# Kernel tuning notes

Measured on AMD Instinct MI355X. Metric: run time of the kernel, lower is better.

## Reference

```python
import jax, jax.numpy as jnp
import numpy as np

EPS = 1e-5
H = 8  # num_heads


def _layernorm(x, g, b):
    m = x.mean(axis=-1, keepdims=True)
    v = jnp.mean((x - m) ** 2, axis=-1, keepdims=True)
    return (x - m) / jnp.sqrt(v + EPS) * g + b


def setup_inputs() -> dict:
    key = jax.random.key(0)
    ks = jax.random.split(key, 8)
    B, T, N, D, L = 4, 4096, 512, 1024, 768
    x = jax.random.normal(ks[0], (B, T, D), dtype=jnp.float32)
    cond = jax.random.normal(ks[1], (B, N, L), dtype=jnp.float32)
    # LayerNorm params
    ln_g = jnp.ones((D,), jnp.float32)
    ln_b = jnp.zeros((D,), jnp.float32)
    tln_g = jnp.ones((L,), jnp.float32)
    tln_b = jnp.zeros((L,), jnp.float32)
    # Linear params, stored as (in, out)
    Wq = jax.random.normal(ks[2], (D, D), jnp.float32) * 0.02
    bq = jnp.zeros((D,), jnp.float32)
    Wk = jax.random.normal(ks[3], (L, D), jnp.float32) * 0.02
    bk = jnp.zeros((D,), jnp.float32)
    Wv = jax.random.normal(ks[4], (L, D), jnp.float32) * 0.02
    bv = jnp.zeros((D,), jnp.float32)
    return {"input_tensor": x, "condition_tensor": cond,
            "ln_g": ln_g, "ln_b": ln_b, "tln_g": tln_g, "tln_b": tln_b,
            "Wq": Wq, "bq": bq, "Wk": Wk, "bk": bk, "Wv": Wv, "bv": bv}


def reference(input_tensor, condition_tensor, ln_g, ln_b, tln_g, tln_b,
              Wq, bq, Wk, bk, Wv, bv):
    B, T, D = input_tensor.shape
    N = condition_tensor.shape[1]
    xn = _layernorm(input_tensor, ln_g, ln_b)            # [B,T,D]
    cn = _layernorm(condition_tensor, tln_g, tln_b)      # [B,N,L]
    q = jnp.einsum('btd,de->bte', xn, Wq) + bq           # [B,T,D]
    k = jnp.einsum('bnl,ld->bnd', cn, Wk) + bk           # [B,N,D]
    v = jnp.einsum('bnl,ld->bnd', cn, Wv) + bv           # [B,N,D]
    q = jax.nn.softmax(q.reshape(B, T, H, D // H), axis=-1)  # softmax over head_dim
    k = jax.nn.softmax(k.reshape(B, N, H, D // H), axis=1)   # softmax over N
    v = v.reshape(B, N, H, D // H)
    context = jnp.einsum('bnhk,bnhv->bhkv', k, v)        # [B,H,hd,hd]
    y = jnp.einsum('bthk,bhkv->bthv', q, context).reshape(B, T, D)
    return y
```

## Files before the change

kernel.cpp:

```cpp
#include <hip/hip_runtime.h>
#include <hip/hip_bf16.h>
#include <stdint.h>

#define BATCH 4
#define TLEN  4096
#define DDIM  1024
#define NCOND 512
#define LDIM  768
#define NHEAD 8
#define HD    128

typedef __bf16 bf16x8 __attribute__((ext_vector_type(8)));
typedef float  f32x4  __attribute__((ext_vector_type(4)));

__device__ __forceinline__ unsigned short f2b(float f) {
    unsigned int u = __builtin_bit_cast(unsigned int, f);
    unsigned int r = (u + 0x7fffu + ((u >> 16) & 1u)) >> 16;
    return (unsigned short)r;
}
__device__ __forceinline__ float b2f(unsigned short s) {
    unsigned int u = ((unsigned int)s) << 16;
    return __builtin_bit_cast(float, u);
}

__device__ __forceinline__ void gl2lds(const void* g, void* l) {
    __builtin_amdgcn_global_load_lds(
        (const __attribute__((address_space(1))) void*)(uintptr_t)g,
        (__attribute__((address_space(3))) void*)(uintptr_t)l,
        16, 0, 0);
}

template<int NCH>
__global__ __launch_bounds__(256) void ln_apply(const float* __restrict__ x,
    const float* __restrict__ g, const float* __restrict__ bb,
    unsigned short* __restrict__ o, int rowlen)
{
    int wid = threadIdx.x >> 6, lane = threadIdx.x & 63;
    long r = (long)blockIdx.x * 4 + wid;
    const float* p = x + r * (long)rowlen;
    float4 v[NCH];
    float s = 0.f, ss = 0.f;
#pragma unroll
    for (int i = 0; i < NCH; i++) {
        v[i] = *(const float4*)(p + i * 256 + lane * 4);
        s  += v[i].x + v[i].y + v[i].z + v[i].w;
        ss += v[i].x * v[i].x + v[i].y * v[i].y + v[i].z * v[i].z + v[i].w * v[i].w;
    }
#pragma unroll
    for (int off = 32; off; off >>= 1) {
        s  += __shfl_xor(s,  off, 64);
        ss += __shfl_xor(ss, off, 64);
    }
    float mu = s / rowlen;
    float rs = rsqrtf(fmaxf(ss / rowlen - mu * mu, 0.f) + 1e-5f);
    unsigned short* po = o + r * (long)rowlen;
#pragma unroll
    for (int i = 0; i < NCH; i++) {
        int c = i * 256 + lane * 4;
        float4 gv = *(const float4*)(g + c);
        float4 bv = *(const float4*)(bb + c);
        ushort4 o4;
        o4.x = f2b((v[i].x - mu) * rs * gv.x + bv.x);
        o4.y = f2b((v[i].y - mu) * rs * gv.y + bv.y);
        o4.z = f2b((v[i].z - mu) * rs * gv.z + bv.z);
        o4.w = f2b((v[i].w - mu) * rs * gv.w + bv.w);
        *(ushort4*)(po + c) = o4;
    }
}

__global__ __launch_bounds__(256) void wtrans(const float* __restrict__ W, int K, int N,
                                              unsigned short* __restrict__ Wt)
{
    __shared__ float t[32][33];
    int n0 = blockIdx.x * 32, k0 = blockIdx.y * 32;
    int tx = threadIdx.x & 31, ty = threadIdx.x >> 5;
#pragma unroll
    for (int i = 0; i < 4; i++)
        t[ty + i * 8][tx] = W[(long)(k0 + ty + i * 8) * N + n0 + tx];
    __syncthreads();
#pragma unroll
    for (int i = 0; i < 4; i++)
        Wt[(long)(n0 + ty + i * 8) * K + k0 + tx] = f2b(t[tx][ty + i * 8]);
}

__global__ __launch_bounds__(256) void gemm_kv(
    const unsigned short* __restrict__ A,
    const unsigned short* __restrict__ Bt,
    const float* __restrict__ bk, const float* __restrict__ bv,
    float* __restrict__ Ck,
    unsigned short* __restrict__ Cvv)
{
    int zi = blockIdx.z;
    const unsigned short* Bp = Bt + (long)zi * 1024 * LDIM;
    const float* bias = zi ? bv : bk;

    int m0 = blockIdx.y * 128, n0 = blockIdx.x * 128;
    int tid = threadIdx.x, lane = tid & 63, wid = tid >> 6;
    int l16 = lane & 15, quad = lane >> 4;
    int mw = (wid & 1) << 6, nw = (wid >> 1) << 6;

    __shared__ unsigned short As[128 * 32];
    __shared__ unsigned short Bs[128 * 32];

    f32x4 acc[4][4];
#pragma unroll
    for (int i = 0; i < 4; i++)
#pragma unroll
        for (int j = 0; j < 4; j++) { acc[i][j][0] = 0.f; acc[i][j][1] = 0.f; acc[i][j][2] = 0.f; acc[i][j][3] = 0.f; }

    const unsigned short* ag = A  + (long)(m0 + (tid >> 2)) * LDIM + (tid & 3) * 8;
    const unsigned short* bg = Bp + (long)(n0 + (tid >> 2)) * LDIM + (tid & 3) * 8;
    unsigned short* asw = As + wid * 512;
    unsigned short* bsw = Bs + wid * 512;
    const long a64 = 64L * LDIM;

    for (int kt = 0; kt < LDIM; kt += 32) {
        gl2lds(ag + kt,        asw);
        gl2lds(ag + a64 + kt,  asw + 2048);
        gl2lds(bg + kt,        bsw);
        gl2lds(bg + a64 + kt,  bsw + 2048);
        __syncthreads();
        bf16x8 af[4], bfr[4];
#pragma unroll
        for (int i = 0; i < 4; i++)
            af[i] = *(const bf16x8*)&As[(mw + i * 16 + l16) * 32 + quad * 8];
#pragma unroll
        for (int j = 0; j < 4; j++)
            bfr[j] = *(const bf16x8*)&Bs[(nw + j * 16 + l16) * 32 + quad * 8];
#pragma unroll
        for (int i = 0; i < 4; i++)
#pragma unroll
            for (int j = 0; j < 4; j++)
                acc[i][j] = __builtin_amdgcn_mfma_f32_16x16x32_bf16(af[i], bfr[j], acc[i][j], 0, 0, 0);
        __syncthreads();
    }

#pragma unroll
    for (int j = 0; j < 4; j++) {
        int col = n0 + nw + j * 16 + l16;
        float bvv = bias[col];
#pragma unroll
        for (int i = 0; i < 4; i++) {
            int row0 = m0 + mw + i * 16 + (quad << 2);
#pragma unroll
            for (int r = 0; r < 4; r++) {
                float val = acc[i][j][r] + bvv;
                long idx = (long)(row0 + r) * DDIM + col;
                if (zi == 0) Ck[idx]  = val;
                else         Cvv[idx] = f2b(val);
            }
        }
    }
}

__global__ __launch_bounds__(256) void kstats(const float* __restrict__ k,
                                              float* __restrict__ Mv,
                                              float* __restrict__ Sv)
{
    int b = blockIdx.x >> 5, chunk = blockIdx.x & 31;
    int c = threadIdx.x & 31;
    int col = chunk * 32 + c;
    int ns  = threadIdx.x >> 5;
    const float* p = k + (long)b * NCOND * DDIM + col;
    float m = -1e30f, s = 0.f;
#pragma unroll 4
    for (int i = 0; i < 64; i++) {
        float v = p[(long)(ns * 64 + i) * DDIM];
        float nm = fmaxf(m, v);
        s = s * __expf(m - nm) + __expf(v - nm);
        m = nm;
    }
    __shared__ float shm[8][33], shs[8][33];
    shm[ns][c] = m; shs[ns][c] = s;
    __syncthreads();
    if (ns == 0) {
        float M = shm[0][c], S = shs[0][c];
#pragma unroll
        for (int t = 1; t < 8; t++) {
            float m2 = shm[t][c], s2 = shs[t][c];
            float nm = fmaxf(M, m2);
            S = S * __expf(M - nm) + s2 * __expf(m2 - nm);
            M = nm;
        }
        Mv[b * DDIM + col] = M;
        Sv[b * DDIM + col] = 1.f / S;
    }
}

__global__ __launch_bounds__(256) void ctx_mfma(const float* __restrict__ kraw,
    const unsigned short* __restrict__ v,
    const float* __restrict__ Mv, const float* __restrict__ Sv,
    float* __restrict__ ctxf)
{
    __shared__ unsigned short kT[128 * 72];
    __shared__ unsigned short vT[128 * 72];
    int s0 = blockIdx.x;
    int bh = blockIdx.y;
    int b = bh >> 3, h = bh & 7;
    int n0 = s0 * 64;
    int tid = threadIdx.x;

    const float* kp = kraw + (long)b * NCOND * DDIM + (long)n0 * DDIM + h * HD;
    const unsigned short* vp = v + (long)b * NCOND * DDIM + (long)n0 * DDIM + h * HD;
    const float* Mp = Mv + b * DDIM + h * HD;
    const float* Sp = Sv + b * DDIM + h * HD;

#pragma unroll 8
    for (int p = 0; p < 32; p++) {
        int e = p * 256 + tid;
        int nn = e >> 7, kk = e & 127;
        float val = __expf(kp[(long)nn * DDIM + kk] - Mp[kk]) * Sp[kk];
        kT[kk * 72 + nn] = f2b(val);
    }
#pragma unroll 8
    for (int p = 0; p < 16; p++) {
        int e = p * 256 + tid;
        int nn = e >> 6, v2 = (e & 63) * 2;
        unsigned int w = *(const unsigned int*)&vp[(long)nn * DDIM + v2];
        vT[v2 * 72 + nn]       = (unsigned short)w;
        vT[(v2 + 1) * 72 + nn] = (unsigned short)(w >> 16);
    }
    __syncthreads();

    int lane = tid & 63, wid = tid >> 6;
    int l16 = lane & 15, quad = lane >> 4;
    int mw = (wid & 1) << 6, nw = (wid >> 1) << 6;
    f32x4 acc[4][4];
#pragma unroll
    for (int i = 0; i < 4; i++)
#pragma unroll
        for (int j = 0; j < 4; j++) { acc[i][j][0] = 0.f; acc[i][j][1] = 0.f; acc[i][j][2] = 0.f; acc[i][j][3] = 0.f; }

#pragma unroll
    for (int ks = 0; ks < 2; ks++) {
        bf16x8 af[4], bfr[4];
#pragma unroll
        for (int i = 0; i < 4; i++)
            af[i] = *(const bf16x8*)&vT[(mw + i * 16 + l16) * 72 + ks * 32 + quad * 8];
#pragma unroll
        for (int j = 0; j < 4; j++)
            bfr[j] = *(const bf16x8*)&kT[(nw + j * 16 + l16) * 72 + ks * 32 + quad * 8];
#pragma unroll
        for (int i = 0; i < 4; i++)
#pragma unroll
            for (int j = 0; j < 4; j++)
                acc[i][j] = __builtin_amdgcn_mfma_f32_16x16x32_bf16(af[i], bfr[j], acc[i][j], 0, 0, 0);
    }

    float* cf = ctxf + ((long)bh << 14);
#pragma unroll
    for (int i = 0; i < 4; i++)
#pragma unroll
        for (int j = 0; j < 4; j++)
#pragma unroll
            for (int r = 0; r < 4; r++)
                atomicAdd(&cf[(mw + i * 16 + quad * 4 + r) * 128 + nw + j * 16 + l16],
                          acc[i][j][r]);
}

__global__ __launch_bounds__(256) void ctxcvt(const float* __restrict__ cf,
                                              unsigned short* __restrict__ ct)
{
    int i = (blockIdx.x * 256 + threadIdx.x) * 4;
    float4 v = *(const float4*)(cf + i);
    ushort4 o;
    o.x = f2b(v.x); o.y = f2b(v.y); o.z = f2b(v.z); o.w = f2b(v.w);
    *(ushort4*)(ct + i) = o;
}

__global__ __launch_bounds__(256, 4) void qfused(
    const unsigned short* __restrict__ xn,
    const unsigned short* __restrict__ wqT,
    const float* __restrict__ bq,
    const unsigned short* __restrict__ ctxT,
    float* __restrict__ out)
{
    __shared__ unsigned short buf[18432];
    unsigned short* As = buf;
    unsigned short* Bs = buf + 4096;
    unsigned short* Pb = buf;
    float* redM = (float*)(buf + 17408);
    float* redS = redM + 256;

    int head = blockIdx.y;
    int m0 = blockIdx.x * 128;
    int b  = m0 >> 12;
    int tid = threadIdx.x, lane = tid & 63, wid = tid >> 6;
    int l16 = lane & 15, quad = lane >> 4;
    int mw = (wid & 1) << 6, nw = (wid >> 1) << 6;
    int ch = wid >> 1;

    const unsigned short* cg = ctxT + ((long)(b * NHEAD + head) << 14);

    f32x4 acc[4][4];
#pragma unroll
    for (int i = 0; i < 4; i++)
#pragma unroll
        for (int j = 0; j < 4; j++) { acc[i][j][0] = 0.f; acc[i][j][1] = 0.f; acc[i][j][2] = 0.f; acc[i][j][3] = 0.f; }

    const unsigned short* ag = xn  + (long)(m0 + (tid >> 2)) * DDIM + (tid & 3) * 8;
    const unsigned short* bg = wqT + (long)(head * 128 + (tid >> 2)) * DDIM + (tid & 3) * 8;
    unsigned short* asw = As + wid * 512;
    unsigned short* bsw = Bs + wid * 512;
    const long a64 = 64L * DDIM;

    for (int kt = 0; kt < DDIM; kt += 32) {
        gl2lds(ag + kt,        asw);
        gl2lds(ag + a64 + kt,  asw + 2048);
        gl2lds(bg + kt,        bsw);
        gl2lds(bg + a64 + kt,  bsw + 2048);
        __syncthreads();
        bf16x8 af[4], bfr[4];
#pragma unroll
        for (int i = 0; i < 4; i++)
            af[i] = *(const bf16x8*)&As[(mw + i * 16 + l16) * 32 + quad * 8];
#pragma unroll
        for (int j = 0; j < 4; j++)
            bfr[j] = *(const bf16x8*)&Bs[(nw + j * 16 + l16) * 32 + quad * 8];
#pragma unroll
        for (int i = 0; i < 4; i++)
#pragma unroll
            for (int j = 0; j < 4; j++)
                acc[i][j] = __builtin_amdgcn_mfma_f32_16x16x32_bf16(af[i], bfr[j], acc[i][j], 0, 0, 0);
        __syncthreads();
    }

    float bvv[4];
#pragma unroll
    for (int j = 0; j < 4; j++) bvv[j] = bq[head * 128 + nw + j * 16 + l16];
#pragma unroll
    for (int i = 0; i < 4; i++)
#pragma unroll
        for (int j = 0; j < 4; j++)
#pragma unroll
            for (int r = 0; r < 4; r++) acc[i][j][r] += bvv[j];

    float mx[4][4];
#pragma unroll
    for (int i = 0; i < 4; i++)
#pragma unroll
        for (int r = 0; r < 4; r++) {
            float m = acc[i][0][r];
            m = fmaxf(m, acc[i][1][r]);
            m = fmaxf(m, acc[i][2][r]);
            m = fmaxf(m, acc[i][3][r]);
            mx[i][r] = m;
        }
#pragma unroll
    for (int off = 1; off < 16; off <<= 1)
#pragma unroll
        for (int i = 0; i < 4; i++)
#pragma unroll
            for (int r = 0; r < 4; r++)
                mx[i][r] = fmaxf(mx[i][r], __shfl_xor(mx[i][r], off, 64));
    if (l16 == 0) {
#pragma unroll
        for (int i = 0; i < 4; i++)
#pragma unroll
            for (int r = 0; r < 4; r++)
                redM[ch * 128 + mw + i * 16 + quad * 4 + r] = mx[i][r];
    }
    __syncthreads();

    float sm[4][4];
#pragma unroll
    for (int i = 0; i < 4; i++)
#pragma unroll
        for (int r = 0; r < 4; r++) {
            int row = mw + i * 16 + quad * 4 + r;
            float M = fmaxf(redM[row], redM[128 + row]);
            float s = 0.f;
#pragma unroll
            for (int j = 0; j < 4; j++) {
                unsigned short eb = f2b(__expf(acc[i][j][r] - M));
                Pb[row * 136 + nw + j * 16 + l16] = eb;
                s += b2f(eb);
            }
            sm[i][r] = s;
        }
#pragma unroll
    for (int off = 1; off < 16; off <<= 1)
#pragma unroll
        for (int i = 0; i < 4; i++)
#pragma unroll
            for (int r = 0; r < 4; r++)
                sm[i][r] += __shfl_xor(sm[i][r], off, 64);
    if (l16 == 0) {
#pragma unroll
        for (int i = 0; i < 4; i++)
#pragma unroll
            for (int r = 0; r < 4; r++)
                redS[ch * 128 + mw + i * 16 + quad * 4 + r] = sm[i][r];
    }
    __syncthreads();

    f32x4 acc2[4][4];
#pragma unroll
    for (int i = 0; i < 4; i++)
#pragma unroll
        for (int j = 0; j < 4; j++) { acc2[i][j][0] = 0.f; acc2[i][j][1] = 0.f; acc2[i][j][2] = 0.f; acc2[i][j][3] = 0.f; }
#pragma unroll
    for (int ks = 0; ks < 4; ks++) {
        bf16x8 af[4], bfr[4];
#pragma unroll
        for (int j = 0; j < 4; j++)
            bfr[j] = *(const bf16x8*)&cg[(nw + j * 16 + l16) * 128 + ks * 32 + quad * 8];
#pragma unroll
        for (int i = 0; i < 4; i++)
            af[i] = *(const bf16x8*)&Pb[(mw + i * 16 + l16) * 136 + ks * 32 + quad * 8];
#pragma unroll
        for (int i = 0; i < 4; i++)
#pragma unroll
            for (int j = 0; j < 4; j++)
                acc2[i][j] = __builtin_amdgcn_mfma_f32_16x16x32_bf16(af[i], bfr[j], acc2[i][j], 0, 0, 0);
    }

#pragma unroll
    for (int i = 0; i < 4; i++)
#pragma unroll
        for (int r = 0; r < 4; r++) {
            int row = mw + i * 16 + quad * 4 + r;
            float invd = 1.f / (redS[row] + redS[128 + row]);
            float* op = out + (long)(m0 + row) * DDIM + head * 128;
#pragma unroll
            for (int j = 0; j < 4; j++)
                op[nw + j * 16 + l16] = acc2[i][j][r] * invd;
        }
}

extern "C" void kernel_launch(void* const* d_in, const int* in_sizes, int n_in,
                              void* d_out, int out_size, void* d_ws, size_t ws_size,
                              hipStream_t stream) {
    (void)in_sizes; (void)n_in; (void)out_size; (void)ws_size;
    const float* x     = (const float*)d_in[0];
    const float* cond  = (const float*)d_in[1];
    const float* ln_g  = (const float*)d_in[2];
    const float* ln_b  = (const float*)d_in[3];
    const float* tln_g = (const float*)d_in[4];
    const float* tln_b = (const float*)d_in[5];
    const float* Wq    = (const float*)d_in[6];
    const float* bq    = (const float*)d_in[7];
    const float* Wk    = (const float*)d_in[8];
    const float* bk    = (const float*)d_in[9];
    const float* Wv    = (const float*)d_in[10];
    const float* bv    = (const float*)d_in[11];
    float* out = (float*)d_out;

    uint8_t* w8 = (uint8_t*)d_ws;
    unsigned short* xn   = (unsigned short*)w8;
    unsigned short* cn   = (unsigned short*)(w8 + 33554432);
    unsigned short* wqT  = (unsigned short*)(w8 + 36700160);
    unsigned short* wkvT = (unsigned short*)(w8 + 38797312);
    float*          fk   = (float*)(w8 + 41943040);
    unsigned short* fvb  = (unsigned short*)(w8 + 50331648);
    float*          ctxf = (float*)(w8 + 54525952);
    unsigned short* ctxT = (unsigned short*)(w8 + 56623104);
    float*          Mv   = (float*)(w8 + 57671680);
    float*          Sv   = (float*)(w8 + 57688064);

    hipMemsetAsync(ctxf, 0, 32 * 128 * 128 * sizeof(float), stream);

    ln_apply<3><<<512, 256, 0, stream>>>(cond, tln_g, tln_b, cn, LDIM);
    wtrans<<<dim3(32, 24), 256, 0, stream>>>(Wk, LDIM, DDIM, wkvT);
    wtrans<<<dim3(32, 24), 256, 0, stream>>>(Wv, LDIM, DDIM, wkvT + 768 * 1024);
    ln_apply<4><<<4096, 256, 0, stream>>>(x, ln_g, ln_b, xn, DDIM);
    wtrans<<<dim3(32, 32), 256, 0, stream>>>(Wq, DDIM, DDIM, wqT);

    gemm_kv<<<dim3(8, 16, 2), 256, 0, stream>>>(cn, wkvT, bk, bv, fk, fvb);

    kstats<<<128, 256, 0, stream>>>(fk, Mv, Sv);
    ctx_mfma<<<dim3(8, 32), 256, 0, stream>>>(fk, fvb, Mv, Sv, ctxf);
    ctxcvt<<<512, 256, 0, stream>>>(ctxf, ctxT);

    qfused<<<dim3(128, 8), 256, 0, stream>>>(xn, wqT, bq, ctxT, out);
}
```

Measured before the change: 272.5 us.

## Double-buffer GEMM LDS loads with XOR swizzle and merge weight transposes

```diff
diff --git a/kernel.cpp b/kernel.cpp
--- a/kernel.cpp
+++ b/kernel.cpp
@@ -68,15 +68,24 @@
     }
 }
 
-__global__ __launch_bounds__(256) void wtrans(const float* __restrict__ W, int K, int N,
-                                              unsigned short* __restrict__ Wt)
-{
+__global__ __launch_bounds__(256) void wtrans3(
+    const float* __restrict__ Wq, const float* __restrict__ Wk,
+    const float* __restrict__ Wv,
+    unsigned short* __restrict__ wqT, unsigned short* __restrict__ wkvT)
+{
+    int z = blockIdx.z;
+    int K = z ? LDIM : DDIM;
+    int k0 = blockIdx.y * 32;
+    if (k0 >= K) return;
+    const float* W = z == 0 ? Wq : (z == 1 ? Wk : Wv);
+    unsigned short* Wt = z == 0 ? wqT : (z == 1 ? wkvT : wkvT + 768 * 1024);
+
     __shared__ float t[32][33];
-    int n0 = blockIdx.x * 32, k0 = blockIdx.y * 32;
+    int n0 = blockIdx.x * 32;
     int tx = threadIdx.x & 31, ty = threadIdx.x >> 5;
 #pragma unroll
     for (int i = 0; i < 4; i++)
-        t[ty + i * 8][tx] = W[(long)(k0 + ty + i * 8) * N + n0 + tx];
+        t[ty + i * 8][tx] = W[(long)(k0 + ty + i * 8) * DDIM + n0 + tx];
     __syncthreads();
 #pragma unroll
     for (int i = 0; i < 4; i++)
@@ -99,8 +108,7 @@
     int l16 = lane & 15, quad = lane >> 4;
     int mw = (wid & 1) << 6, nw = (wid >> 1) << 6;
 
-    __shared__ unsigned short As[128 * 32];
-    __shared__ unsigned short Bs[128 * 32];
+    __shared__ unsigned short sb[16384];
 
     f32x4 acc[4][4];
 #pragma unroll
@@ -108,31 +116,45 @@
 #pragma unroll
         for (int j = 0; j < 4; j++) { acc[i][j][0] = 0.f; acc[i][j][1] = 0.f; acc[i][j][2] = 0.f; acc[i][j][3] = 0.f; }
 
-    const unsigned short* ag = A  + (long)(m0 + (tid >> 2)) * LDIM + (tid & 3) * 8;
-    const unsigned short* bg = Bp + (long)(n0 + (tid >> 2)) * LDIM + (tid & 3) * 8;
-    unsigned short* asw = As + wid * 512;
-    unsigned short* bsw = Bs + wid * 512;
+    int cg = (tid & 3) ^ ((tid >> 3) & 3);
+    const unsigned short* ag = A  + (long)(m0 + (tid >> 2)) * LDIM + cg * 8;
+    const unsigned short* bg = Bp + (long)(n0 + (tid >> 2)) * LDIM + cg * 8;
     const long a64 = 64L * LDIM;
-
-    for (int kt = 0; kt < LDIM; kt += 32) {
-        gl2lds(ag + kt,        asw);
-        gl2lds(ag + a64 + kt,  asw + 2048);
-        gl2lds(bg + kt,        bsw);
-        gl2lds(bg + a64 + kt,  bsw + 2048);
-        __syncthreads();
+    int wsl = wid * 512;
+    int sw = (l16 >> 1) & 3;
+
+    auto stage = [&](unsigned short* d, int ko) {
+        gl2lds(ag + ko,        d + wsl);
+        gl2lds(ag + a64 + ko,  d + wsl + 2048);
+        gl2lds(bg + ko,        d + 4096 + wsl);
+        gl2lds(bg + a64 + ko,  d + 4096 + wsl + 2048);
+    };
+
+    const int NT = LDIM >> 5;
+    stage(sb, 0);
+    stage(sb + 8192, 32);
+
+    for (int t = 0; t < NT; ++t) {
+        if (t + 1 < NT) asm volatile("s_waitcnt vmcnt(4)" ::: "memory");
+        else            asm volatile("s_waitcnt vmcnt(0)" ::: "memory");
+        __builtin_amdgcn_s_barrier();
+        __builtin_amdgcn_sched_barrier(0);
+        unsigned short* Ac = sb + (t & 1) * 8192;
         bf16x8 af[4], bfr[4];
 #pragma unroll
         for (int i = 0; i < 4; i++)
-            af[i] = *(const bf16x8*)&As[(mw + i * 16 + l16) * 32 + quad * 8];
+            af[i] = *(const bf16x8*)&Ac[(mw + i * 16 + l16) * 32 + ((quad ^ sw) * 8)];
 #pragma unroll
         for (int j = 0; j < 4; j++)
-            bfr[j] = *(const bf16x8*)&Bs[(nw + j * 16 + l16) * 32 + quad * 8];
+            bfr[j] = *(const bf16x8*)&Ac[4096 + (nw + j * 16 + l16) * 32 + ((quad ^ sw) * 8)];
 #pragma unroll
         for (int i = 0; i < 4; i++)
 #pragma unroll
             for (int j = 0; j < 4; j++)
                 acc[i][j] = __builtin_amdgcn_mfma_f32_16x16x32_bf16(af[i], bfr[j], acc[i][j], 0, 0, 0);
-        __syncthreads();
+        __builtin_amdgcn_s_barrier();
+        __builtin_amdgcn_sched_barrier(0);
+        if (t + 2 < NT) stage(Ac, (t + 2) << 5);
     }
 
 #pragma unroll
@@ -276,8 +298,6 @@
     float* __restrict__ out)
 {
     __shared__ unsigned short buf[18432];
-    unsigned short* As = buf;
-    unsigned short* Bs = buf + 4096;
     unsigned short* Pb = buf;
     float* redM = (float*)(buf + 17408);
     float* redS = redM + 256;
@@ -290,7 +310,7 @@
     int mw = (wid & 1) << 6, nw = (wid >> 1) << 6;
     int ch = wid >> 1;
 
-    const unsigned short* cg = ctxT + ((long)(b * NHEAD + head) << 14);
+    const unsigned short* cg2 = ctxT + ((long)(b * NHEAD + head) << 14);
 
     f32x4 acc[4][4];
 #pragma unroll
@@ -298,31 +318,45 @@
 #pragma unroll
         for (int j = 0; j < 4; j++) { acc[i][j][0] = 0.f; acc[i][j][1] = 0.f; acc[i][j][2] = 0.f; acc[i][j][3] = 0.f; }
 
-    const unsigned short* ag = xn  + (long)(m0 + (tid >> 2)) * DDIM + (tid & 3) * 8;
-    const unsigned short* bg = wqT + (long)(head * 128 + (tid >> 2)) * DDIM + (tid & 3) * 8;
-    unsigned short* asw = As + wid * 512;
-    unsigned short* bsw = Bs + wid * 512;
+    int cgs = (tid & 3) ^ ((tid >> 3) & 3);
+    const unsigned short* ag = xn  + (long)(m0 + (tid >> 2)) * DDIM + cgs * 8;
+    const unsigned short* bg = wqT + (long)(head * 128 + (tid >> 2)) * DDIM + cgs * 8;
     const long a64 = 64L * DDIM;
-
-    for (int kt = 0; kt < DDIM; kt += 32) {
-        gl2lds(ag + kt,        asw);
-        gl2lds(ag + a64 + kt,  asw + 2048);
-        gl2lds(bg + kt,        bsw);
-        gl2lds(bg + a64 + kt,  bsw + 2048);
-        __syncthreads();
+    int wsl = wid * 512;
+    int sw = (l16 >> 1) & 3;
+
+    auto stage = [&](unsigned short* d, int ko) {
+        gl2lds(ag + ko,        d + wsl);
+        gl2lds(ag + a64 + ko,  d + wsl + 2048);
+        gl2lds(bg + ko,        d + 4096 + wsl);
+        gl2lds(bg + a64 + ko,  d + 4096 + wsl + 2048);
+    };
+
+    const int NT = DDIM >> 5;
+    stage(buf, 0);
+    stage(buf + 8192, 32);
+
+    for (int t = 0; t < NT; ++t) {
+        if (t + 1 < NT) asm volatile("s_waitcnt vmcnt(4)" ::: "memory");
+        else            asm volatile("s_waitcnt vmcnt(0)" ::: "memory");
+        __builtin_amdgcn_s_barrier();
+        __builtin_amdgcn_sched_barrier(0);
+        unsigned short* Ac = buf + (t & 1) * 8192;
         bf16x8 af[4], bfr[4];
 #pragma unroll
         for (int i = 0; i < 4; i++)
-            af[i] = *(const bf16x8*)&As[(mw + i * 16 + l16) * 32 + quad * 8];
+            af[i] = *(const bf16x8*)&Ac[(mw + i * 16 + l16) * 32 + ((quad ^ sw) * 8)];
 #pragma unroll
         for (int j = 0; j < 4; j++)
-            bfr[j] = *(const bf16x8*)&Bs[(nw + j * 16 + l16) * 32 + quad * 8];
+            bfr[j] = *(const bf16x8*)&Ac[4096 + (nw + j * 16 + l16) * 32 + ((quad ^ sw) * 8)];
 #pragma unroll
         for (int i = 0; i < 4; i++)
 #pragma unroll
             for (int j = 0; j < 4; j++)
                 acc[i][j] = __builtin_amdgcn_mfma_f32_16x16x32_bf16(af[i], bfr[j], acc[i][j], 0, 0, 0);
-        __syncthreads();
+        __builtin_amdgcn_s_barrier();
+        __builtin_amdgcn_sched_barrier(0);
+        if (t + 2 < NT) stage(Ac, (t + 2) << 5);
     }
 
     float bvv[4];
@@ -404,7 +438,7 @@
         bf16x8 af[4], bfr[4];
 #pragma unroll
         for (int j = 0; j < 4; j++)
-            bfr[j] = *(const bf16x8*)&cg[(nw + j * 16 + l16) * 128 + ks * 32 + quad * 8];
+            bfr[j] = *(const bf16x8*)&cg2[(nw + j * 16 + l16) * 128 + ks * 32 + quad * 8];
 #pragma unroll
         for (int i = 0; i < 4; i++)
             af[i] = *(const bf16x8*)&Pb[(mw + i * 16 + l16) * 136 + ks * 32 + quad * 8];
@@ -461,10 +495,8 @@
     hipMemsetAsync(ctxf, 0, 32 * 128 * 128 * sizeof(float), stream);
 
     ln_apply<3><<<512, 256, 0, stream>>>(cond, tln_g, tln_b, cn, LDIM);
-    wtrans<<<dim3(32, 24), 256, 0, stream>>>(Wk, LDIM, DDIM, wkvT);
-    wtrans<<<dim3(32, 24), 256, 0, stream>>>(Wv, LDIM, DDIM, wkvT + 768 * 1024);
     ln_apply<4><<<4096, 256, 0, stream>>>(x, ln_g, ln_b, xn, DDIM);
-    wtrans<<<dim3(32, 32), 256, 0, stream>>>(Wq, DDIM, DDIM, wqT);
+    wtrans3<<<dim3(32, 32, 3), 256, 0, stream>>>(Wq, Wk, Wv, wqT, wkvT);
 
     gemm_kv<<<dim3(8, 16, 2), 256, 0, stream>>>(cn, wkvT, bk, bv, fk, fvb);
 
```

Measured after the change: 254.7 us. 1.07x faster.
